# Kernel tuning notes

Measured on AMD Instinct MI355X. Metric: run time of the kernel, lower is better.

Reference implementation:

```python
import jax, jax.numpy as jnp
import numpy as np

TEMPERATURE = 1.0
NUM_EXPERTS = 8


def setup_inputs() -> dict:
    key = jax.random.key(0)
    ks = jax.random.split(key, 7)
    B, S, H, E = 4, 4096, 1024, NUM_EXPERTS
    scale = 1.0 / np.sqrt(H)
    return {
        "hidden_states": jax.random.normal(ks[0], (B, S, H), dtype=jnp.float32),
        "w1": jax.random.normal(ks[1], (H, H // 2), dtype=jnp.float32) * scale,
        "b1": jax.random.normal(ks[2], (H // 2,), dtype=jnp.float32) * 0.01,
        "w2": jax.random.normal(ks[3], (H // 2, E), dtype=jnp.float32) * (1.0 / np.sqrt(H // 2)),
        "b2": jax.random.normal(ks[4], (E,), dtype=jnp.float32) * 0.01,
        "expert_W": jax.random.normal(ks[5], (E, H, H), dtype=jnp.float32) * scale,
        "expert_b": jax.random.normal(ks[6], (E, H), dtype=jnp.float32) * 0.01,
    }


def reference(hidden_states, w1, b1, w2, b2, expert_W, expert_b):
    # Router MLP: Linear(H, H//2) -> ReLU -> Linear(H//2, E)  (dropout inactive at eval)
    h = jax.nn.relu(jnp.einsum("bsh,hm->bsm", hidden_states, w1) + b1)
    routing_scores = (jnp.einsum("bsm,me->bse", h, w2) + b2) / TEMPERATURE
    expert_probs = jax.nn.softmax(routing_scores, axis=-1)
    # top-1 routing (topk with k=1 == argmax of probs)
    top_idx = jnp.argmax(expert_probs, axis=-1)  # [B, S]
    onehot = jax.nn.one_hot(top_idx, NUM_EXPERTS, dtype=hidden_states.dtype)  # [B, S, E]

    # _apply_expert_routing: for each expert, masked input -> dense transform -> masked accumulate
    routed = jnp.zeros_like(hidden_states)
    for e in range(NUM_EXPERTS):
        mask = onehot[..., e:e + 1]  # [B, S, 1]
        expert_out = jnp.einsum("bsh,hd->bsd", hidden_states * mask, expert_W[e]) + expert_b[e]
        routed = routed + expert_out * mask
    return routed
```

## Files before the change

kernel.cpp:

```cpp
#include <hip/hip_runtime.h>

#define NTOK 16384
#define HDIM 1024
#define MDIM 512
#define NEXP 8
#define CHUNK 128
#define MAXCHUNK 136
#define RCAP 4096
#define DELTA 0.02f
#define LSTR 72

typedef __bf16 bf16x8 __attribute__((ext_vector_type(8)));
typedef float floatx4 __attribute__((ext_vector_type(4)));

__device__ __forceinline__ void gll16(const void* g, void* l) {
  __builtin_amdgcn_global_load_lds(
      (const __attribute__((address_space(1))) void*)g,
      (__attribute__((address_space(3))) void*)l, 16, 0, 0);
}

__global__ __launch_bounds__(256) void cvt_hs(
    const float* __restrict__ src, __bf16* __restrict__ dst)
{
  const size_t i = ((size_t)blockIdx.x * 256 + threadIdx.x) * 8;
  float4 a = *(const float4*)&src[i];
  float4 b = *(const float4*)&src[i + 4];
  bf16x8 o;
  o[0] = (__bf16)a.x; o[1] = (__bf16)a.y; o[2] = (__bf16)a.z; o[3] = (__bf16)a.w;
  o[4] = (__bf16)b.x; o[5] = (__bf16)b.y; o[6] = (__bf16)b.z; o[7] = (__bf16)b.w;
  *(bf16x8*)&dst[i] = o;
}

__global__ __launch_bounds__(256) void transpose_cvt(
    const float* __restrict__ src, __bf16* __restrict__ dst, int K, int C)
{
  __shared__ __align__(16) __bf16 T[64 * LSTR];
  const int b = blockIdx.z;
  const int k0 = blockIdx.x * 64, c0 = blockIdx.y * 64;
  const float* S = src + (size_t)b * K * C;
  __bf16* D = dst + (size_t)b * K * C;
  const int t = threadIdx.x;
  {
    const int r = t >> 2, cc = (t & 3) * 16;
    const float* p = S + (size_t)(k0 + r) * C + c0 + cc;
    float4 v0 = *(const float4*)&p[0];
    float4 v1 = *(const float4*)&p[4];
    float4 v2 = *(const float4*)&p[8];
    float4 v3 = *(const float4*)&p[12];
    float vv[16] = {v0.x, v0.y, v0.z, v0.w, v1.x, v1.y, v1.z, v1.w,
                    v2.x, v2.y, v2.z, v2.w, v3.x, v3.y, v3.z, v3.w};
#pragma unroll
    for (int j = 0; j < 16; ++j) T[(cc + j) * LSTR + r] = (__bf16)vv[j];
  }
  __syncthreads();
  {
    const int c = t >> 2, kk = (t & 3) * 16;
    __bf16* q = D + (size_t)(c0 + c) * K + k0 + kk;
    *(float4*)&q[0] = *(const float4*)&T[c * LSTR + kk];
    *(float4*)&q[8] = *(const float4*)&T[c * LSTR + kk + 8];
  }
}

__global__ __launch_bounds__(256) void gemm1_score(
    const __bf16* __restrict__ A,
    const __bf16* __restrict__ Bt,
    const float* __restrict__ bias,
    const float* __restrict__ w2,
    float* __restrict__ scores_part)
{
  __shared__ __align__(16) __bf16 As[128 * 64];
  __shared__ __align__(16) __bf16 Bs[128 * 64];

  const int tid = threadIdx.x;
  const int row0 = blockIdx.y * 128, col0 = blockIdx.x * 128;
  const int wave = tid >> 6, lane = tid & 63;
  const int lrow8 = lane >> 3;
  const int gchunk = (lane & 7) ^ lrow8;
  const int wr = (wave >> 1) * 64, wc = (wave & 1) * 64;
  const int lrow = lane & 15, quad = lane >> 4;

  const __bf16 *pa[4], *pb[4];
#pragma unroll
  for (int p = 0; p < 4; ++p) {
    const int rb = wave * 8 + p * 32;
    pa[p] = A + (size_t)(row0 + rb + lrow8) * HDIM + gchunk * 8;
    pb[p] = Bt + (size_t)(col0 + rb + lrow8) * HDIM + gchunk * 8;
  }

  floatx4 acc[4][4];
#pragma unroll
  for (int i = 0; i < 4; ++i)
#pragma unroll
    for (int j = 0; j < 4; ++j) acc[i][j] = (floatx4){0.f, 0.f, 0.f, 0.f};

  for (int k0 = 0; k0 < HDIM; k0 += 64) {
#pragma unroll
    for (int p = 0; p < 4; ++p) {
      const int rb = wave * 8 + p * 32;
      gll16(pa[p] + k0, &As[rb * 64]);
      gll16(pb[p] + k0, &Bs[rb * 64]);
    }
    __syncthreads();
#pragma unroll
    for (int kh = 0; kh < 2; ++kh) {
      bf16x8 a[4], b[4];
#pragma unroll
      for (int i = 0; i < 4; ++i)
        a[i] = *(const bf16x8*)&As[(wr + i * 16 + lrow) * 64 +
                                   (((kh * 4 + quad) ^ (lrow & 7)) * 8)];
#pragma unroll
      for (int j = 0; j < 4; ++j)
        b[j] = *(const bf16x8*)&Bs[(wc + j * 16 + lrow) * 64 +
                                   (((kh * 4 + quad) ^ (lrow & 7)) * 8)];
#pragma unroll
      for (int i = 0; i < 4; ++i)
#pragma unroll
        for (int j = 0; j < 4; ++j)
          acc[i][j] = __builtin_amdgcn_mfma_f32_16x16x32_bf16(a[i], b[j], acc[i][j], 0, 0, 0);
    }
    __syncthreads();
  }

  float* w2s = (float*)As;
  float* sblk = (float*)Bs;
  *(float4*)&w2s[tid * 4] = *(const float4*)&w2[col0 * 8 + tid * 4];
  __syncthreads();

  float bj[4];
  float4 wja[4], wjb[4];
#pragma unroll
  for (int j = 0; j < 4; ++j) {
    const int cl = wc + j * 16 + lrow;
    bj[j] = bias[col0 + cl];
    wja[j] = *(const float4*)&w2s[cl * 8];
    wjb[j] = *(const float4*)&w2s[cl * 8 + 4];
  }

#pragma unroll
  for (int i = 0; i < 4; ++i) {
#pragma unroll
    for (int r = 0; r < 4; ++r) {
      float4 sA = {0, 0, 0, 0}, sB = {0, 0, 0, 0};
#pragma unroll
      for (int j = 0; j < 4; ++j) {
        float h = fmaxf(acc[i][j][r] + bj[j], 0.f);
        sA.x += h * wja[j].x; sA.y += h * wja[j].y;
        sA.z += h * wja[j].z; sA.w += h * wja[j].w;
        sB.x += h * wjb[j].x; sB.y += h * wjb[j].y;
        sB.z += h * wjb[j].z; sB.w += h * wjb[j].w;
      }
#pragma unroll
      for (int m = 1; m <= 8; m <<= 1) {
        sA.x += __shfl_xor(sA.x, m, 64); sA.y += __shfl_xor(sA.y, m, 64);
        sA.z += __shfl_xor(sA.z, m, 64); sA.w += __shfl_xor(sA.w, m, 64);
        sB.x += __shfl_xor(sB.x, m, 64); sB.y += __shfl_xor(sB.y, m, 64);
        sB.z += __shfl_xor(sB.z, m, 64); sB.w += __shfl_xor(sB.w, m, 64);
      }
      if (lrow == 0) {
        const int rloc = wr + i * 16 + quad * 4 + r;
        *(float4*)&sblk[((wave & 1) * 128 + rloc) * 8] = sA;
        *(float4*)&sblk[((wave & 1) * 128 + rloc) * 8 + 4] = sB;
      }
    }
  }
  __syncthreads();
  {
    const int r = tid >> 1, e4 = (tid & 1) * 4;
    float4 v0 = *(const float4*)&sblk[r * 8 + e4];
    float4 v1 = *(const float4*)&sblk[(128 + r) * 8 + e4];
    float4 o = {v0.x + v1.x, v0.y + v1.y, v0.z + v1.z, v0.w + v1.w};
    *(float4*)&scores_part[((size_t)blockIdx.x * NTOK + row0 + r) * 8 + e4] = o;
  }
}

__global__ __launch_bounds__(256) void routing_argmax(
    const float* __restrict__ scores_part, const float* __restrict__ b2,
    int* __restrict__ top_idx, int* __restrict__ risky_n,
    int* __restrict__ risky)
{
  __shared__ int rbuf[256];
  __shared__ int rcnt, rbase;
  if (threadIdx.x == 0) rcnt = 0;
  __syncthreads();

  const int t = blockIdx.x * 256 + threadIdx.x;
  float4 sa = {0, 0, 0, 0}, sb = {0, 0, 0, 0};
#pragma unroll
  for (int c = 0; c < 4; ++c) {
    float4 va = *(const float4*)&scores_part[((size_t)c * NTOK + t) * 8];
    float4 vb = *(const float4*)&scores_part[((size_t)c * NTOK + t) * 8 + 4];
    sa.x += va.x; sa.y += va.y; sa.z += va.z; sa.w += va.w;
    sb.x += vb.x; sb.y += vb.y; sb.z += vb.z; sb.w += vb.w;
  }
  float s[8] = {sa.x + b2[0], sa.y + b2[1], sa.z + b2[2], sa.w + b2[3],
                sb.x + b2[4], sb.y + b2[5], sb.z + b2[6], sb.w + b2[7]};
  float best = s[0], second = -1e30f;
  int bi = 0;
#pragma unroll
  for (int e = 1; e < 8; ++e) {
    if (s[e] > best) { second = best; best = s[e]; bi = e; }
    else if (s[e] > second) second = s[e];
  }
  top_idx[t] = bi;
  if (best - second < DELTA) rbuf[atomicAdd(&rcnt, 1)] = t;
  __syncthreads();
  if (threadIdx.x == 0 && rcnt > 0) rbase = atomicAdd(risky_n, rcnt);
  __syncthreads();
  if ((int)threadIdx.x < rcnt) {
    int slot = rbase + threadIdx.x;
    if (slot < RCAP) risky[slot] = rbuf[threadIdx.x];
  }
}

__global__ __launch_bounds__(256) void gemm1_fix_v2(
    const float* __restrict__ A, const float* __restrict__ W,
    const float* __restrict__ bias, const int* __restrict__ risky,
    float* __restrict__ hfix)
{
  __shared__ float As[32][33];
  __shared__ float Bs[32][64];
  __shared__ int toks[32];

  const int tid = threadIdx.x;
  if (tid < 32) toks[tid] = risky[blockIdx.y * 32 + tid];
  __syncthreads();
  if (toks[0] < 0) return;

  const int col0 = blockIdx.x * 64;
  const int tx = tid & 15, ty = tid >> 4;
  float acc0[4] = {0, 0, 0, 0}, acc1[4] = {0, 0, 0, 0};

  const int sr = tid >> 3;
  const int sc4 = (tid & 3) * 8;
  const int lo = tid & 7;
  const int sc8 = lo * 8;
  const int tokS = toks[sr];
  const float* pa = (tokS >= 0) ? A + (size_t)tokS * HDIM : A;

  for (int k0 = 0; k0 < HDIM; k0 += 32) {
    float4 av = make_float4(0, 0, 0, 0);
    if (tokS >= 0) av = *(const float4*)&pa[k0 + (lo & 3) * 4 + (lo >> 2) * 16];
    float4 b0 = *(const float4*)&W[(size_t)(k0 + sr) * MDIM + col0 + sc8];
    float4 b1v = *(const float4*)&W[(size_t)(k0 + sr) * MDIM + col0 + sc8 + 4];
    const int kk = (lo & 3) * 4 + (lo >> 2) * 16;
    As[kk + 0][sr] = av.x; As[kk + 1][sr] = av.y;
    As[kk + 2][sr] = av.z; As[kk + 3][sr] = av.w;
    (void)sc4;
    *(float4*)&Bs[sr][sc8] = b0;
    *(float4*)&Bs[sr][sc8 + 4] = b1v;
    __syncthreads();

#pragma unroll
    for (int k = 0; k < 32; ++k) {
      float a0 = As[k][ty], a1 = As[k][ty + 16];
      float4 bv = *(const float4*)&Bs[k][tx * 4];
      acc0[0] = fmaf(a0, bv.x, acc0[0]); acc0[1] = fmaf(a0, bv.y, acc0[1]);
      acc0[2] = fmaf(a0, bv.z, acc0[2]); acc0[3] = fmaf(a0, bv.w, acc0[3]);
      acc1[0] = fmaf(a1, bv.x, acc1[0]); acc1[1] = fmaf(a1, bv.y, acc1[1]);
      acc1[2] = fmaf(a1, bv.z, acc1[2]); acc1[3] = fmaf(a1, bv.w, acc1[3]);
    }
    __syncthreads();
  }

  const int c = col0 + tx * 4;
  const int i0 = blockIdx.y * 32 + ty, i1 = blockIdx.y * 32 + ty + 16;
  if (toks[ty] >= 0) {
    float4 v;
    v.x = fmaxf(acc0[0] + bias[c + 0], 0.f); v.y = fmaxf(acc0[1] + bias[c + 1], 0.f);
    v.z = fmaxf(acc0[2] + bias[c + 2], 0.f); v.w = fmaxf(acc0[3] + bias[c + 3], 0.f);
    *(float4*)&hfix[(size_t)i0 * MDIM + c] = v;
  }
  if (toks[ty + 16] >= 0) {
    float4 v;
    v.x = fmaxf(acc1[0] + bias[c + 0], 0.f); v.y = fmaxf(acc1[1] + bias[c + 1], 0.f);
    v.z = fmaxf(acc1[2] + bias[c + 2], 0.f); v.w = fmaxf(acc1[3] + bias[c + 3], 0.f);
    *(float4*)&hfix[(size_t)i1 * MDIM + c] = v;
  }
}

__global__ __launch_bounds__(256) void rescore_fix(
    const float* __restrict__ hfix, const float* __restrict__ w2,
    const float* __restrict__ b2, const int* __restrict__ risky,
    int* __restrict__ top_idx)
{
  const int idx = blockIdx.x * 32 + (threadIdx.x >> 3);
  const int l8 = threadIdx.x & 7;
  const int t = risky[idx];

  float s[8] = {0, 0, 0, 0, 0, 0, 0, 0};
  if (t >= 0) {
    const float* hrow = hfix + (size_t)idx * MDIM;
    for (int k = l8; k < MDIM; k += 8) {
      float hv = hrow[k];
      float4 wa = *(const float4*)&w2[k * 8];
      float4 wb = *(const float4*)&w2[k * 8 + 4];
      s[0] += hv * wa.x; s[1] += hv * wa.y; s[2] += hv * wa.z; s[3] += hv * wa.w;
      s[4] += hv * wb.x; s[5] += hv * wb.y; s[6] += hv * wb.z; s[7] += hv * wb.w;
    }
  }
#pragma unroll
  for (int off = 4; off > 0; off >>= 1)
#pragma unroll
    for (int e = 0; e < 8; ++e) s[e] += __shfl_xor(s[e], off, 64);

  if (l8 == 0 && t >= 0) {
    float best = s[0] + b2[0];
    int bi = 0;
#pragma unroll
    for (int e = 1; e < 8; ++e) {
      float v = s[e] + b2[e];
      if (v > best) { best = v; bi = e; }
    }
    top_idx[t] = bi;
  }
}

__global__ __launch_bounds__(256) void count_tokens(
    const int* __restrict__ top_idx, int* __restrict__ counts)
{
  __shared__ int lc[NEXP];
  if (threadIdx.x < NEXP) lc[threadIdx.x] = 0;
  __syncthreads();
  atomicAdd(&lc[top_idx[blockIdx.x * 256 + threadIdx.x]], 1);
  __syncthreads();
  if (threadIdx.x < NEXP) atomicAdd(&counts[threadIdx.x], lc[threadIdx.x]);
}

__global__ __launch_bounds__(256) void scatter_tokens(
    const int* __restrict__ top_idx, const int* __restrict__ counts,
    int* __restrict__ cursor, int* __restrict__ sorted)
{
  __shared__ int lc[NEXP], lbase[NEXP], off_s[NEXP];
  if (threadIdx.x < NEXP) lc[threadIdx.x] = 0;
  if (threadIdx.x == 0) {
    int off = 0;
    for (int e = 0; e < NEXP; ++e) {
      off_s[e] = off;
      off += ((counts[e] + CHUNK - 1) / CHUNK) * CHUNK;
    }
  }
  __syncthreads();
  const int t = blockIdx.x * 256 + threadIdx.x;
  const int e = top_idx[t];
  const int r = atomicAdd(&lc[e], 1);
  __syncthreads();
  if (threadIdx.x < NEXP)
    lbase[threadIdx.x] = atomicAdd(&cursor[threadIdx.x], lc[threadIdx.x]);
  __syncthreads();
  sorted[off_s[e] + lbase[e] + r] = t;
}

__global__ __launch_bounds__(256) void expert_gemm_v3(
    const __bf16* __restrict__ A,
    const __bf16* __restrict__ Wt,
    const float* __restrict__ Eb,
    const int* __restrict__ sorted,
    const int* __restrict__ top_idx,
    float* __restrict__ Out)
{
  __shared__ __align__(16) __bf16 As[128 * 64];
  __shared__ __align__(16) __bf16 Bs[128 * 64];
  __shared__ int toks[CHUNK];

  const int tid = threadIdx.x;
  if (tid < CHUNK) toks[tid] = sorted[(size_t)blockIdx.y * CHUNK + tid];
  __syncthreads();
  if (toks[0] < 0) return;

  const int e = top_idx[toks[0]];
  const int col0 = blockIdx.x * 128;
  const int wave = tid >> 6, lane = tid & 63;
  const int lrow8 = lane >> 3;
  const int gchunk = (lane & 7) ^ lrow8;
  const int wr = (wave >> 1) * 64, wc = (wave & 1) * 64;
  const int lrow = lane & 15, quad = lane >> 4;

  const __bf16 *pa[4], *pb[4];
#pragma unroll
  for (int p = 0; p < 4; ++p) {
    const int rb = wave * 8 + p * 32;
    const int tk = toks[rb + lrow8];
    pa[p] = A + (size_t)(tk < 0 ? 0 : tk) * HDIM + gchunk * 8;
    pb[p] = Wt + ((size_t)e * HDIM + col0 + rb + lrow8) * HDIM + gchunk * 8;
  }

  floatx4 acc[4][4];
#pragma unroll
  for (int i = 0; i < 4; ++i)
#pragma unroll
    for (int j = 0; j < 4; ++j) acc[i][j] = (floatx4){0.f, 0.f, 0.f, 0.f};

  for (int k0 = 0; k0 < HDIM; k0 += 64) {
#pragma unroll
    for (int p = 0; p < 4; ++p) {
      const int rb = wave * 8 + p * 32;
      gll16(pa[p] + k0, &As[rb * 64]);
      gll16(pb[p] + k0, &Bs[rb * 64]);
    }
    __syncthreads();
#pragma unroll
    for (int kh = 0; kh < 2; ++kh) {
      bf16x8 a[4], b[4];
#pragma unroll
      for (int i = 0; i < 4; ++i)
        a[i] = *(const bf16x8*)&As[(wr + i * 16 + lrow) * 64 +
                                   (((kh * 4 + quad) ^ (lrow & 7)) * 8)];
#pragma unroll
      for (int j = 0; j < 4; ++j)
        b[j] = *(const bf16x8*)&Bs[(wc + j * 16 + lrow) * 64 +
                                   (((kh * 4 + quad) ^ (lrow & 7)) * 8)];
#pragma unroll
      for (int i = 0; i < 4; ++i)
#pragma unroll
        for (int j = 0; j < 4; ++j)
          acc[i][j] = __builtin_amdgcn_mfma_f32_16x16x32_bf16(a[i], b[j], acc[i][j], 0, 0, 0);
    }
    __syncthreads();
  }

  const float* be = Eb + (size_t)e * HDIM + col0;
#pragma unroll
  for (int i = 0; i < 4; ++i)
#pragma unroll
    for (int r = 0; r < 4; ++r) {
      const int row = wr + i * 16 + quad * 4 + r;
      const int tok = toks[row];
      if (tok < 0) continue;
      float* po = Out + (size_t)tok * HDIM + col0;
#pragma unroll
      for (int j = 0; j < 4; ++j) {
        const int col = wc + j * 16 + lrow;
        po[col] = acc[i][j][r] + be[col];
      }
    }
}

extern "C" void kernel_launch(void* const* d_in, const int* in_sizes, int n_in,
                              void* d_out, int out_size, void* d_ws, size_t ws_size,
                              hipStream_t stream) {
  (void)in_sizes; (void)n_in; (void)out_size; (void)ws_size;

  const float* hs = (const float*)d_in[0];
  const float* w1 = (const float*)d_in[1];
  const float* b1 = (const float*)d_in[2];
  const float* w2 = (const float*)d_in[3];
  const float* b2 = (const float*)d_in[4];
  const float* eW = (const float*)d_in[5];
  const float* eb = (const float*)d_in[6];
  float* out = (float*)d_out;

  float* hfix = (float*)d_out;
  float* scores_part = hfix + (size_t)RCAP * MDIM;

  char* wsb = (char*)d_ws;
  int* top_idx = (int*)wsb;
  int* ctrl    = (int*)(wsb + 65536);
  int* counts  = ctrl;
  int* risky_n = ctrl + 8;
  int* cursor  = ctrl + 16;
  int* risky   = (int*)(wsb + 65792);
  int* sorted  = risky + RCAP;
  __bf16* hs_bf = (__bf16*)(wsb + 163840);
  __bf16* w1t   = (__bf16*)(wsb + 163840 + 33554432);
  __bf16* eWt   = (__bf16*)(wsb + 163840 + 33554432 + 1048576);

  hipMemsetAsync(ctrl, 0, 128, stream);
  hipMemsetAsync(risky, 0xFF, (RCAP + MAXCHUNK * CHUNK) * sizeof(int), stream);

  cvt_hs<<<NTOK * HDIM / (256 * 8), 256, 0, stream>>>(hs, hs_bf);
  transpose_cvt<<<dim3(HDIM / 64, MDIM / 64, 1), 256, 0, stream>>>(w1, w1t, HDIM, MDIM);
  transpose_cvt<<<dim3(HDIM / 64, HDIM / 64, NEXP), 256, 0, stream>>>(eW, eWt, HDIM, HDIM);

  gemm1_score<<<dim3(MDIM / 128, NTOK / 128), 256, 0, stream>>>(hs_bf, w1t, b1, w2, scores_part);
  routing_argmax<<<NTOK / 256, 256, 0, stream>>>(scores_part, b2, top_idx, risky_n, risky);
  gemm1_fix_v2<<<dim3(MDIM / 64, RCAP / 32), 256, 0, stream>>>(hs, w1, b1, risky, hfix);
  rescore_fix<<<RCAP / 32, 256, 0, stream>>>(hfix, w2, b2, risky, top_idx);
  count_tokens<<<NTOK / 256, 256, 0, stream>>>(top_idx, counts);
  scatter_tokens<<<NTOK / 256, 256, 0, stream>>>(top_idx, counts, cursor, sorted);
  expert_gemm_v3<<<dim3(HDIM / 128, MAXCHUNK), 256, 0, stream>>>(hs_bf, eWt, eb, sorted, top_idx, out);
}
```

Before: 329.1 us.

## Double-buffer LDS tiles and remap workgroups in router and expert GEMMs

Both the router GEMM and the expert GEMM now use two LDS buffers, so the global-to-LDS load of the next K tile is issued before computing on the current one, which removes one barrier per iteration. Launches become 1D grids with a swizzled block-to-tile mapping that spreads consecutive workgroups across XCDs while keeping tiles that share A rows grouped, aiming for better L2 reuse. LDS use doubles to 64KB per block, which may lower occupancy.

```diff
diff --git a/kernel.cpp b/kernel.cpp
--- a/kernel.cpp
+++ b/kernel.cpp
@@ -9,6 +9,9 @@
 #define RCAP 4096
 #define DELTA 0.02f
 #define LSTR 72
+
+#define G1_NWG ((MDIM / 128) * (NTOK / 128))
+#define EG_NWG (8 * MAXCHUNK)
 
 typedef __bf16 bf16x8 __attribute__((ext_vector_type(8)));
 typedef float floatx4 __attribute__((ext_vector_type(4)));
@@ -68,11 +71,14 @@
     const float* __restrict__ w2,
     float* __restrict__ scores_part)
 {
-  __shared__ __align__(16) __bf16 As[128 * 64];
-  __shared__ __align__(16) __bf16 Bs[128 * 64];
+  __shared__ __align__(16) __bf16 As[2 * 128 * 64];
+  __shared__ __align__(16) __bf16 Bs[2 * 128 * 64];
 
   const int tid = threadIdx.x;
-  const int row0 = blockIdx.y * 128, col0 = blockIdx.x * 128;
+  const int swz = (blockIdx.x & 7) * (G1_NWG / 8) + (blockIdx.x >> 3);
+  const int rowBlk = swz >> 2;
+  const int cb = swz & 3;
+  const int row0 = rowBlk * 128, col0 = cb * 128;
   const int wave = tid >> 6, lane = tid & 63;
   const int lrow8 = lane >> 3;
   const int gchunk = (lane & 7) ^ lrow8;
@@ -93,24 +99,38 @@
 #pragma unroll
     for (int j = 0; j < 4; ++j) acc[i][j] = (floatx4){0.f, 0.f, 0.f, 0.f};
 
-  for (int k0 = 0; k0 < HDIM; k0 += 64) {
-#pragma unroll
-    for (int p = 0; p < 4; ++p) {
-      const int rb = wave * 8 + p * 32;
-      gll16(pa[p] + k0, &As[rb * 64]);
-      gll16(pb[p] + k0, &Bs[rb * 64]);
-    }
-    __syncthreads();
+#pragma unroll
+  for (int p = 0; p < 4; ++p) {
+    const int rb = wave * 8 + p * 32;
+    gll16(pa[p], &As[rb * 64]);
+    gll16(pb[p], &Bs[rb * 64]);
+  }
+  __syncthreads();
+
+  int cur = 0;
+  for (int t = 0; t < HDIM / 64; ++t) {
+    const int nxt = cur ^ 1;
+    if (t + 1 < HDIM / 64) {
+      const int koff = (t + 1) * 64;
+#pragma unroll
+      for (int p = 0; p < 4; ++p) {
+        const int rb = wave * 8 + p * 32;
+        gll16(pa[p] + koff, &As[nxt * 8192 + rb * 64]);
+        gll16(pb[p] + koff, &Bs[nxt * 8192 + rb * 64]);
+      }
+    }
+    const __bf16* Ab = &As[cur * 8192];
+    const __bf16* Bb = &Bs[cur * 8192];
 #pragma unroll
     for (int kh = 0; kh < 2; ++kh) {
       bf16x8 a[4], b[4];
 #pragma unroll
       for (int i = 0; i < 4; ++i)
-        a[i] = *(const bf16x8*)&As[(wr + i * 16 + lrow) * 64 +
+        a[i] = *(const bf16x8*)&Ab[(wr + i * 16 + lrow) * 64 +
                                    (((kh * 4 + quad) ^ (lrow & 7)) * 8)];
 #pragma unroll
       for (int j = 0; j < 4; ++j)
-        b[j] = *(const bf16x8*)&Bs[(wc + j * 16 + lrow) * 64 +
+        b[j] = *(const bf16x8*)&Bb[(wc + j * 16 + lrow) * 64 +
                                    (((kh * 4 + quad) ^ (lrow & 7)) * 8)];
 #pragma unroll
       for (int i = 0; i < 4; ++i)
@@ -119,6 +139,7 @@
           acc[i][j] = __builtin_amdgcn_mfma_f32_16x16x32_bf16(a[i], b[j], acc[i][j], 0, 0, 0);
     }
     __syncthreads();
+    cur = nxt;
   }
 
   float* w2s = (float*)As;
@@ -169,7 +190,7 @@
     float4 v0 = *(const float4*)&sblk[r * 8 + e4];
     float4 v1 = *(const float4*)&sblk[(128 + r) * 8 + e4];
     float4 o = {v0.x + v1.x, v0.y + v1.y, v0.z + v1.z, v0.w + v1.w};
-    *(float4*)&scores_part[((size_t)blockIdx.x * NTOK + row0 + r) * 8 + e4] = o;
+    *(float4*)&scores_part[((size_t)cb * NTOK + row0 + r) * 8 + e4] = o;
   }
 }
 
@@ -350,7 +371,7 @@
   sorted[off_s[e] + lbase[e] + r] = t;
 }
 
-__global__ __launch_bounds__(256) void expert_gemm_v3(
+__global__ __launch_bounds__(256) void expert_gemm_v4(
     const __bf16* __restrict__ A,
     const __bf16* __restrict__ Wt,
     const float* __restrict__ Eb,
@@ -358,17 +379,20 @@
     const int* __restrict__ top_idx,
     float* __restrict__ Out)
 {
-  __shared__ __align__(16) __bf16 As[128 * 64];
-  __shared__ __align__(16) __bf16 Bs[128 * 64];
+  __shared__ __align__(16) __bf16 As[2 * 128 * 64];
+  __shared__ __align__(16) __bf16 Bs[2 * 128 * 64];
   __shared__ int toks[CHUNK];
 
   const int tid = threadIdx.x;
-  if (tid < CHUNK) toks[tid] = sorted[(size_t)blockIdx.y * CHUNK + tid];
+  const int swz = (blockIdx.x & 7) * (EG_NWG / 8) + (blockIdx.x >> 3);
+  const int chunkIdx = swz >> 3;
+  const int cb = swz & 7;
+  if (tid < CHUNK) toks[tid] = sorted[(size_t)chunkIdx * CHUNK + tid];
   __syncthreads();
   if (toks[0] < 0) return;
 
   const int e = top_idx[toks[0]];
-  const int col0 = blockIdx.x * 128;
+  const int col0 = cb * 128;
   const int wave = tid >> 6, lane = tid & 63;
   const int lrow8 = lane >> 3;
   const int gchunk = (lane & 7) ^ lrow8;
@@ -390,24 +414,38 @@
 #pragma unroll
     for (int j = 0; j < 4; ++j) acc[i][j] = (floatx4){0.f, 0.f, 0.f, 0.f};
 
-  for (int k0 = 0; k0 < HDIM; k0 += 64) {
-#pragma unroll
-    for (int p = 0; p < 4; ++p) {
-      const int rb = wave * 8 + p * 32;
-      gll16(pa[p] + k0, &As[rb * 64]);
-      gll16(pb[p] + k0, &Bs[rb * 64]);
-    }
-    __syncthreads();
+#pragma unroll
+  for (int p = 0; p < 4; ++p) {
+    const int rb = wave * 8 + p * 32;
+    gll16(pa[p], &As[rb * 64]);
+    gll16(pb[p], &Bs[rb * 64]);
+  }
+  __syncthreads();
+
+  int cur = 0;
+  for (int t = 0; t < HDIM / 64; ++t) {
+    const int nxt = cur ^ 1;
+    if (t + 1 < HDIM / 64) {
+      const int koff = (t + 1) * 64;
+#pragma unroll
+      for (int p = 0; p < 4; ++p) {
+        const int rb = wave * 8 + p * 32;
+        gll16(pa[p] + koff, &As[nxt * 8192 + rb * 64]);
+        gll16(pb[p] + koff, &Bs[nxt * 8192 + rb * 64]);
+      }
+    }
+    const __bf16* Ab = &As[cur * 8192];
+    const __bf16* Bb = &Bs[cur * 8192];
 #pragma unroll
     for (int kh = 0; kh < 2; ++kh) {
       bf16x8 a[4], b[4];
 #pragma unroll
       for (int i = 0; i < 4; ++i)
-        a[i] = *(const bf16x8*)&As[(wr + i * 16 + lrow) * 64 +
+        a[i] = *(const bf16x8*)&Ab[(wr + i * 16 + lrow) * 64 +
                                    (((kh * 4 + quad) ^ (lrow & 7)) * 8)];
 #pragma unroll
       for (int j = 0; j < 4; ++j)
-        b[j] = *(const bf16x8*)&Bs[(wc + j * 16 + lrow) * 64 +
+        b[j] = *(const bf16x8*)&Bb[(wc + j * 16 + lrow) * 64 +
                                    (((kh * 4 + quad) ^ (lrow & 7)) * 8)];
 #pragma unroll
       for (int i = 0; i < 4; ++i)
@@ -416,6 +454,7 @@
           acc[i][j] = __builtin_amdgcn_mfma_f32_16x16x32_bf16(a[i], b[j], acc[i][j], 0, 0, 0);
     }
     __syncthreads();
+    cur = nxt;
   }
 
   const float* be = Eb + (size_t)e * HDIM + col0;
@@ -471,11 +510,11 @@
   transpose_cvt<<<dim3(HDIM / 64, MDIM / 64, 1), 256, 0, stream>>>(w1, w1t, HDIM, MDIM);
   transpose_cvt<<<dim3(HDIM / 64, HDIM / 64, NEXP), 256, 0, stream>>>(eW, eWt, HDIM, HDIM);
 
-  gemm1_score<<<dim3(MDIM / 128, NTOK / 128), 256, 0, stream>>>(hs_bf, w1t, b1, w2, scores_part);
+  gemm1_score<<<dim3(G1_NWG), 256, 0, stream>>>(hs_bf, w1t, b1, w2, scores_part);
   routing_argmax<<<NTOK / 256, 256, 0, stream>>>(scores_part, b2, top_idx, risky_n, risky);
   gemm1_fix_v2<<<dim3(MDIM / 64, RCAP / 32), 256, 0, stream>>>(hs, w1, b1, risky, hfix);
   rescore_fix<<<RCAP / 32, 256, 0, stream>>>(hfix, w2, b2, risky, top_idx);
   count_tokens<<<NTOK / 256, 256, 0, stream>>>(top_idx, counts);
   scatter_tokens<<<NTOK / 256, 256, 0, stream>>>(top_idx, counts, cursor, sorted);
-  expert_gemm_v3<<<dim3(HDIM / 128, MAXCHUNK), 256, 0, stream>>>(hs_bf, eWt, eb, sorted, top_idx, out);
-}
+  expert_gemm_v4<<<dim3(EG_NWG), 256, 0, stream>>>(hs_bf, eWt, eb, sorted, top_idx, out);
+}
```

New measurement: 326.0 us. No clear change (-0.9%).
